# Performance work log

Hardware: AMD Instinct MI355X
Metric: run time of the kernel (lower is better)

## Reference

```python
import jax, jax.numpy as jnp
import numpy as np

B, M, N, K = 64, 1024, 1024, 128

def setup_inputs() -> dict:
    key = jax.random.key(0)
    k1, k2, k3 = jax.random.split(key, 3)
    # int8 operands (stored as int32 per spec; values fit in int8 range)
    a = jax.random.randint(k1, (B, M, K), 0, 127, dtype=jnp.int32)
    b = jax.random.randint(k2, (B, N, K), 0, 127, dtype=jnp.int32)  # S8N: N-major, matmul uses b^T
    alpha = jax.random.uniform(k3, (1,), dtype=jnp.float32) * 0.01
    return {"a": a, "b": b, "alpha": alpha}

def reference(a, b, alpha):
    acc = jnp.einsum('bmk,bnk->bmn', a, b)  # int32 accumulator
    # fused dequant epilogue: scale by alpha, cast to fp16
    return (alpha[0] * acc.astype(jnp.float32)).astype(jnp.float16)
```

## Files before the change

kernel.cpp:

```cpp
#include <hip/hip_runtime.h>


#define Mdim 1024
#define Ndim 1024
#define Kdim 128
#define NROWS 16
#define NSTRIPS 16
#define BSTRIDE 128

using int32x4 = __attribute__((ext_vector_type(4))) int;
using floatx4 = __attribute__((ext_vector_type(4))) float;

__device__ __forceinline__ unsigned pack8(int32x4 v) {
    return (unsigned)(v.x & 255) | ((unsigned)(v.y & 255) << 8)
         | ((unsigned)(v.z & 255) << 16) | ((unsigned)(v.w & 255) << 24);
}

__device__ __forceinline__ int swz(int byte_off) {
    return byte_off ^ (((byte_off >> 7) & 7) << 4);
}

__global__ __launch_bounds__(512, 2)
void bmm_s8_kernel(const int* __restrict__ A, const int* __restrict__ Bm,
                   const float* __restrict__ alpha_p, float* __restrict__ out)
{
    __shared__ unsigned char Bs[1024 * BSTRIDE];

    const int t    = threadIdx.x;
    const int z    = blockIdx.x;
    const int q    = blockIdx.y;
    const int lane = t & 63;
    const int wave = t >> 6;
    const int wn   = wave * 128;

    const int* __restrict__ Ab = A  + (size_t)z * Mdim * Kdim + (size_t)(q * 256) * Kdim;
    const int* __restrict__ Bb = Bm + (size_t)z * Ndim * Kdim;
    float* __restrict__ Ob     = out + (size_t)z * Mdim * Ndim + (size_t)(q * 256) * Ndim;

    const int r = lane & 15;
    const int g = lane >> 4;

    int32x4 araw[8];
#pragma unroll
    for (int k = 0; k < 8; ++k) {
        const int ks = k >> 2, i = k & 3;
        araw[k] = *(const int32x4*)(Ab + (size_t)r * Kdim + ks * 64 + g * 16 + i * 4);
    }

#pragma unroll 1
    for (int rr = 0; rr < 4; ++rr) {
        int32x4 breg[16];
#pragma unroll
        for (int j = 0; j < 16; ++j) {
            const int f    = t + 512 * (rr * 16 + j);
            const int row  = f >> 5;
            const int colb = (f & 31) * 4;
            breg[j] = *(const int32x4*)(Bb + (size_t)row * Kdim + colb);
        }
#pragma unroll
        for (int j = 0; j < 16; ++j) {
            const int f    = t + 512 * (rr * 16 + j);
            const int row  = f >> 5;
            const int colb = (f & 31) * 4;
            *(unsigned*)(&Bs[swz(row * BSTRIDE + colb)]) = pack8(breg[j]);
        }
    }
    __syncthreads();

    const float alpha = alpha_p[0];
    const int cm = lane & 15;
    const int cn = (lane >> 4) * 4;

#pragma unroll 1
    for (int s = 0; s < NSTRIPS; ++s) {
        int32x4 af[2];
#pragma unroll
        for (int ks = 0; ks < 2; ++ks)
            af[ks] = (int32x4){ (int)pack8(araw[ks * 4 + 0]), (int)pack8(araw[ks * 4 + 1]),
                                (int)pack8(araw[ks * 4 + 2]), (int)pack8(araw[ks * 4 + 3]) };

        if (s + 1 < NSTRIPS) {
            const int* __restrict__ An = Ab + (size_t)((s + 1) * NROWS) * Kdim;
#pragma unroll
            for (int k = 0; k < 8; ++k) {
                const int ks = k >> 2, i = k & 3;
                araw[k] = *(const int32x4*)(An + (size_t)r * Kdim + ks * 64 + g * 16 + i * 4);
            }
        }

        int32x4 acc[8];
#pragma unroll
        for (int nt = 0; nt < 8; ++nt)
            acc[nt] = (int32x4){0, 0, 0, 0};

#pragma unroll
        for (int ks = 0; ks < 2; ++ks) {
#pragma unroll
            for (int nt = 0; nt < 8; ++nt) {
                const int row = wn + nt * 16 + r;
                int32x4 bf = *(const int32x4*)(&Bs[swz(row * BSTRIDE + ks * 64 + g * 16)]);
                acc[nt] = __builtin_amdgcn_mfma_i32_16x16x64_i8(bf, af[ks], acc[nt], 0, 0, 0);
            }
        }

        const size_t rowbase = (size_t)(s * NROWS + cm) * Ndim + wn;
#pragma unroll
        for (int nt = 0; nt < 8; ++nt) {
            floatx4 v;
            v.x = alpha * (float)acc[nt][0];
            v.y = alpha * (float)acc[nt][1];
            v.z = alpha * (float)acc[nt][2];
            v.w = alpha * (float)acc[nt][3];
            *(floatx4*)(Ob + rowbase + nt * 16 + cn) = v;
        }

        __syncthreads();
    }
}

extern "C" void kernel_launch(void* const* d_in, const int* in_sizes, int n_in,
                              void* d_out, int out_size, void* d_ws, size_t ws_size,
                              hipStream_t stream) {
    const int*   a     = (const int*)d_in[0];
    const int*   b     = (const int*)d_in[1];
    const float* alpha = (const float*)d_in[2];
    float*       out   = (float*)d_out;

    const int batch = in_sizes[0] / (Mdim * Kdim);
    dim3 grid(batch, Mdim / (NROWS * NSTRIPS));
    bmm_s8_kernel<<<grid, 512, 0, stream>>>(a, b, alpha, out);
}
```

Before: 343.5 us.

## Stage epilogue tiles through LDS for coalesced nontemporal row stores

Each strip's scaled fp32 accumulators are written into a swizzled 16KB LDS buffer four rows at a time, then read back so that each block writes whole contiguous output rows using nontemporal stores. The aim is to replace the MFMA-layout scattered 16-byte global stores with fully coalesced row writes that bypass cache. In exchange it adds LDS traffic, eight extra barriers per strip and more LDS use, which may lower occupancy given the already large 128KB B buffer.

```diff
diff --git a/kernel.cpp b/kernel.cpp
--- a/kernel.cpp
+++ b/kernel.cpp
@@ -20,11 +20,17 @@
     return byte_off ^ (((byte_off >> 7) & 7) << 4);
 }
 
+__device__ __forceinline__ void lds_barrier() {
+    asm volatile("s_waitcnt lgkmcnt(0)\n\ts_barrier" ::: "memory");
+}
+
 __global__ __launch_bounds__(512, 2)
 void bmm_s8_kernel(const int* __restrict__ A, const int* __restrict__ Bm,
                    const float* __restrict__ alpha_p, float* __restrict__ out)
 {
     __shared__ unsigned char Bs[1024 * BSTRIDE];
+    __shared__ int32x4 Cs4[1024];
+    unsigned char* const Cs = (unsigned char*)Cs4;
 
     const int t    = threadIdx.x;
     const int z    = blockIdx.x;
@@ -68,8 +74,6 @@
     __syncthreads();
 
     const float alpha = alpha_p[0];
-    const int cm = lane & 15;
-    const int cn = (lane >> 4) * 4;
 
 #pragma unroll 1
     for (int s = 0; s < NSTRIPS; ++s) {
@@ -103,18 +107,38 @@
             }
         }
 
-        const size_t rowbase = (size_t)(s * NROWS + cm) * Ndim + wn;
+        floatx4 facc[8];
 #pragma unroll
         for (int nt = 0; nt < 8; ++nt) {
-            floatx4 v;
-            v.x = alpha * (float)acc[nt][0];
-            v.y = alpha * (float)acc[nt][1];
-            v.z = alpha * (float)acc[nt][2];
-            v.w = alpha * (float)acc[nt][3];
-            *(floatx4*)(Ob + rowbase + nt * 16 + cn) = v;
+            facc[nt].x = alpha * (float)acc[nt][0];
+            facc[nt].y = alpha * (float)acc[nt][1];
+            facc[nt].z = alpha * (float)acc[nt][2];
+            facc[nt].w = alpha * (float)acc[nt][3];
         }
 
-        __syncthreads();
+#pragma unroll
+        for (int c = 0; c < 4; ++c) {
+            if ((r >> 2) == c) {
+                const int rowL = r & 3;
+                const int xo   = (rowL & 3) << 4;
+#pragma unroll
+                for (int nt = 0; nt < 8; ++nt) {
+                    const int off = rowL * 4096 + wn * 4 + nt * 64 + g * 16;
+                    *(floatx4*)(&Cs[off ^ xo]) = facc[nt];
+                }
+            }
+            lds_barrier();
+
+            const size_t basef = (size_t)(s * NROWS + c * 4) * Ndim;
+#pragma unroll
+            for (int p = 0; p < 2; ++p) {
+                const int off  = (t + p * 512) * 16;
+                const int rowL = off >> 12;
+                floatx4 v = *(const floatx4*)(&Cs[off ^ ((rowL & 3) << 4)]);
+                __builtin_nontemporal_store(v, (floatx4*)(Ob + basef + (off >> 2)));
+            }
+            lds_barrier();
+        }
     }
 }
 
```

After: 330.6 us. -3.8%, faster.
